# Performance work log

Hardware: AMD Instinct MI355X
Metric: run time of the kernel (lower is better)

## Reference

```python
import jax, jax.numpy as jnp
import numpy as np
from itertools import permutations

BLOCK = 64  # GroupLinear block_size


def _dist_bucket_table():
    # replicates self.distance: log2-style bucketing of token distances [0,1024)
    t = np.zeros(1024, dtype=np.int32)
    for i, th in enumerate([2, 4, 8, 16, 32, 64, 128, 256, 512]):
        t[th:] = i + 1
    return jnp.asarray(t)


def setup_inputs() -> dict:
    key = jax.random.key(0)
    ks = jax.random.split(key, 12)
    B, S, H, NH = 4, 512, 768, 12
    E, TAG, TE, TD, R = 24, 7, 20, 20, 97
    DIN = 2 * H + TE + TD
    hidden_state = jax.random.normal(ks[0], (B, S, H), jnp.float32)
    attention = jax.random.uniform(ks[1], (B, NH, S, S), jnp.float32)
    attention_mask = jnp.ones((B, S), jnp.float32)
    head = jnp.sort(jax.random.randint(ks[2], (B, E), 0, S), axis=-1)
    tail = jnp.sort(jax.random.randint(ks[3], (B, E), 0, S), axis=-1)
    entity_type = jax.random.randint(ks[4], (B, E), 0, TAG)
    type_table = jax.random.normal(ks[5], (TAG, TE), jnp.float32) * 0.02
    dis_table = jax.random.normal(ks[6], (20, TD), jnp.float32) * 0.02
    Wh = jax.random.normal(ks[7], (DIN, H), jnp.float32) * (1.0 / np.sqrt(DIN))
    bh = jnp.zeros((H,), jnp.float32)
    Wt = jax.random.normal(ks[8], (DIN, H), jnp.float32) * (1.0 / np.sqrt(DIN))
    bt = jnp.zeros((H,), jnp.float32)
    # GroupLinear weight reshaped to [n_blocks, BLOCK, BLOCK, R]
    clsW = jax.random.normal(ks[9], (H // BLOCK, BLOCK, BLOCK, R), jnp.float32) * (1.0 / np.sqrt(H * BLOCK))
    clsb = jnp.zeros((R,), jnp.float32)
    return dict(hidden_state=hidden_state, attention=attention,
                attention_mask=attention_mask, head=head, tail=tail,
                entity_type=entity_type, type_table=type_table,
                dis_table=dis_table, Wh=Wh, bh=bh, Wt=Wt, bt=bt,
                clsW=clsW, clsb=clsb)


def reference(hidden_state, attention, attention_mask, head, tail, entity_type,
              type_table, dis_table, Wh, bh, Wt, bt, clsW, clsb):
    E = head.shape[1]
    hts = jnp.asarray(list(permutations(range(E), 2)), dtype=jnp.int32)  # [P,2]
    i0, i1 = hts[:, 0], hts[:, 1]
    dtab = _dist_bucket_table()
    att = attention.sum(axis=1)  # [B,S,S] sum over heads

    def per_sample(h, a, m, hd, tl, et):
        # h:[S,H] a:[S,S] m:[S] hd,tl,et:[E]
        ent_feat = (h[hd] + h[tl]) * 0.5          # [E,H]
        ent_att = (a[hd] + a[tl]) * 0.5           # [E,S]
        ent_tf = type_table[et]                   # [E,TE]
        head_f, tail_f = ent_feat[i0], ent_feat[i1]      # [P,H]
        ht_att = ent_att[i0] * ent_att[i1] * m[None, :]  # [P,S]
        head_ty, tail_ty = ent_tf[i0], ent_tf[i1]        # [P,TE]
        d = dtab[jnp.abs(tl[i0] - hd[i1])]               # [P]
        ht_dist = dis_table[d]                           # [P,TD]
        ht_att = ht_att / (ht_att.sum(-1, keepdims=True) + 1e-20)
        ht_info = ht_att @ h                             # [P,H]
        all_h = jnp.concatenate([head_f, ht_info, head_ty, ht_dist], axis=-1)
        all_t = jnp.concatenate([tail_f, ht_info, tail_ty, ht_dist], axis=-1)
        return all_h, all_t

    all_h, all_t = jax.vmap(per_sample)(hidden_state, att, attention_mask,
                                        head, tail, entity_type)
    all_h = all_h.reshape(-1, all_h.shape[-1])  # [B*P, DIN]
    all_t = all_t.reshape(-1, all_t.shape[-1])
    h1 = jnp.tanh(all_h @ Wh + bh)              # [L,H]
    t1 = jnp.tanh(all_t @ Wt + bt)
    L, H = h1.shape
    nb = H // BLOCK
    x1 = h1.reshape(L, nb, BLOCK)
    x2 = t1.reshape(L, nb, BLOCK)
    # GroupLinear: per-block outer product then linear, fused as einsum
    logits = jnp.einsum('lnb,lnc,nbcr->lr', x1, x2, clsW) + clsb  # [L,R]
    return logits
```

## Files before the change

### kernel.cpp

```cpp
#include <hip/hip_runtime.h>
#include <hip/hip_bf16.h>
#include <math.h>

#define B_ 4
#define S_ 512
#define H_ 768
#define NH_ 12
#define E_ 24
#define TE_ 20
#define TD_ 20
#define R_ 97
#define DIN_ 1576
#define KPAD_ 1600
#define KS_MLP 50
#define MF_MLP 140
#define KS_HTI 16
#define P_ 552
#define L_ 2208
#define NB_ 12
#define NF_ 7

typedef __bf16 bf16x8 __attribute__((ext_vector_type(8)));
typedef float f32x4 __attribute__((ext_vector_type(4)));

__device__ __forceinline__ unsigned short f2bf(float f) {
  union { float f; unsigned u; } c; c.f = f;
  unsigned r = c.u + 0x7FFF + ((c.u >> 16) & 1);
  return (unsigned short)(r >> 16);
}
__device__ __forceinline__ float bf2f(unsigned short b) {
  union { unsigned u; float f; } c; c.u = ((unsigned)b) << 16;
  return c.f;
}
__device__ __forceinline__ unsigned pk2(float a, float b) {
  return (unsigned)f2bf(a) | ((unsigned)f2bf(b) << 16);
}
__device__ __forceinline__ void gload_lds16(const uint4* g, uint4* l) {
  __builtin_amdgcn_global_load_lds(
      (const __attribute__((address_space(1))) unsigned*)(const void*)g,
      (__attribute__((address_space(3))) unsigned*)(void*)l, 16, 0, 0);
}

__global__ void ent_prep(const float* __restrict__ attn, const float* __restrict__ hs,
                         const int* __restrict__ head, const int* __restrict__ tail,
                         float* __restrict__ ent_att, float* __restrict__ ent_feat) {
  int be = blockIdx.x;
  int b = be / E_;
  int hd = head[be], tl = tail[be];
  int tid = threadIdx.x;
  const float* abase = attn + (size_t)b * NH_ * S_ * S_;
  for (int s = tid; s < S_; s += 256) {
    float acc = 0.f;
#pragma unroll
    for (int nh = 0; nh < NH_; ++nh) {
      const float* ap = abase + (size_t)nh * S_ * S_;
      acc += ap[(size_t)hd * S_ + s] + ap[(size_t)tl * S_ + s];
    }
    ent_att[(size_t)be * S_ + s] = 0.5f * acc;
  }
  const float* hb = hs + (size_t)b * S_ * H_;
  for (int k = tid; k < H_; k += 256) {
    ent_feat[(size_t)be * H_ + k] = 0.5f * (hb[(size_t)hd * H_ + k] + hb[(size_t)tl * H_ + k]);
  }
}

__global__ void pair_att(const float* __restrict__ ent_att, const float* __restrict__ mask,
                         const int* __restrict__ head, const int* __restrict__ tail,
                         const int* __restrict__ etype,
                         float* __restrict__ ht_att, int* __restrict__ meta) {
  int l = blockIdx.x;
  int b = l / P_, p = l % P_;
  int i0 = p / (E_ - 1), rem = p % (E_ - 1);
  int i1 = rem + (rem >= i0 ? 1 : 0);
  int tid = threadIdx.x;
  if (tid == 0) {
    meta[0 * L_ + l] = b * E_ + i0;
    meta[1 * L_ + l] = b * E_ + i1;
    meta[2 * L_ + l] = etype[b * E_ + i0];
    meta[3 * L_ + l] = etype[b * E_ + i1];
    int d = abs(tail[b * E_ + i0] - head[b * E_ + i1]);
    int bk = (d >= 2) + (d >= 4) + (d >= 8) + (d >= 16) + (d >= 32) +
             (d >= 64) + (d >= 128) + (d >= 256) + (d >= 512);
    meta[4 * L_ + l] = bk;
  }
  const float* a0 = ent_att + (size_t)(b * E_ + i0) * S_;
  const float* a1 = ent_att + (size_t)(b * E_ + i1) * S_;
  const float* m = mask + (size_t)b * S_;
  float v0 = a0[tid] * a1[tid] * m[tid];
  float v1 = a0[tid + 256] * a1[tid + 256] * m[tid + 256];
  float loc = v0 + v1;
  for (int o = 32; o > 0; o >>= 1) loc += __shfl_down(loc, o, 64);
  __shared__ float red[4];
  if ((tid & 63) == 0) red[tid >> 6] = loc;
  __syncthreads();
  float tot = red[0] + red[1] + red[2] + red[3];
  float inv = 1.f / (tot + 1e-20f);
  ht_att[(size_t)l * S_ + tid] = v0 * inv;
  ht_att[(size_t)l * S_ + tid + 256] = v1 * inv;
}

__global__ void pack_hs(const float* __restrict__ hs, uint4* __restrict__ hsP) {
  int u = blockIdx.x * 256 + threadIdx.x;
  if (u >= B_ * KS_HTI * 48 * 64) return;
  int lane = u & 63;
  int t = u >> 6;
  int nt16 = t % 48;
  int t2 = t / 48;
  int ks = t2 % KS_HTI;
  int b = t2 / KS_HTI;
  int n = nt16 * 16 + (lane & 15);
  int k0 = ks * 32 + ((lane >> 4) << 3);
  const float* src = hs + (size_t)b * S_ * H_;
  unsigned w[4];
#pragma unroll
  for (int q = 0; q < 4; ++q) {
    int k = k0 + 2 * q;
    w[q] = pk2(src[(size_t)k * H_ + n], src[(size_t)(k + 1) * H_ + n]);
  }
  uint4 o; o.x = w[0]; o.y = w[1]; o.z = w[2]; o.w = w[3];
  hsP[u] = o;
}

__global__ void pack_Wmlp(const float* __restrict__ Wh, const float* __restrict__ Wt,
                          uint4* __restrict__ WpH, uint4* __restrict__ WpT) {
  int u = blockIdx.x * 256 + threadIdx.x;
  if (u >= KS_MLP * 48 * 64) return;
  const float* W = blockIdx.y ? Wt : Wh;
  uint4* Wp = blockIdx.y ? WpT : WpH;
  int lane = u & 63;
  int t = u >> 6;
  int nt16 = t % 48;
  int ks = t / 48;
  int n = nt16 * 16 + (lane & 15);
  int k0 = ks * 32 + ((lane >> 4) << 3);
  unsigned w[4];
#pragma unroll
  for (int q = 0; q < 4; ++q) {
    int k = k0 + 2 * q;
    float v0 = (k < DIN_) ? W[(size_t)k * H_ + n] : 0.f;
    float v1 = (k + 1 < DIN_) ? W[(size_t)(k + 1) * H_ + n] : 0.f;
    w[q] = pk2(v0, v1);
  }
  uint4 o; o.x = w[0]; o.y = w[1]; o.z = w[2]; o.w = w[3];
  Wp[u] = o;
}

__global__ void pack_allx(const float* __restrict__ ent_feat, const float* __restrict__ ht_info,
                          const float* __restrict__ ttab, const float* __restrict__ dtab,
                          const int* __restrict__ meta,
                          uint4* __restrict__ axH, uint4* __restrict__ axT) {
  int idx = blockIdx.x * 256 + threadIdx.x;
  int lane = idx & 63;
  int unit = idx >> 6;
  int half = unit / (MF_MLP * KS_MLP);
  int rem = unit % (MF_MLP * KS_MLP);
  int mf = rem / KS_MLP, ks = rem % KS_MLP;
  int row = mf * 16 + (lane & 15);
  int k = ks * 32 + ((lane >> 4) << 3);
  uint4 d; d.x = d.y = d.z = d.w = 0;
  if (row < L_) {
    int frow = meta[half * L_ + row];
    int trow = meta[(2 + half) * L_ + row];
    int db = meta[4 * L_ + row];
    if (k < 768) {
      const float* p = ent_feat + (size_t)frow * H_ + k;
      float4 v0 = *(const float4*)p, v1 = *(const float4*)(p + 4);
      d.x = pk2(v0.x, v0.y); d.y = pk2(v0.z, v0.w);
      d.z = pk2(v1.x, v1.y); d.w = pk2(v1.z, v1.w);
    } else if (k < 1536) {
      const float* p = ht_info + (size_t)row * H_ + (k - 768);
      float4 v0 = *(const float4*)p, v1 = *(const float4*)(p + 4);
      d.x = pk2(v0.x, v0.y); d.y = pk2(v0.z, v0.w);
      d.z = pk2(v1.x, v1.y); d.w = pk2(v1.z, v1.w);
    } else {
      float v[8];
#pragma unroll
      for (int j = 0; j < 8; ++j) {
        int e = k + j;
        v[j] = (e < 1556) ? ttab[trow * TE_ + (e - 1536)]
             : (e < 1576) ? dtab[db * TD_ + (e - 1556)] : 0.f;
      }
      d.x = pk2(v[0], v[1]); d.y = pk2(v[2], v[3]);
      d.z = pk2(v[4], v[5]); d.w = pk2(v[6], v[7]);
    }
  }
  (half ? axT : axH)[(size_t)rem * 64 + lane] = d;
}

__global__ __launch_bounds__(256) void htinfo_mfma(
    const float* __restrict__ htatt, const uint4* __restrict__ hsP,
    float* __restrict__ htinfo) {
  int b = blockIdx.z;
  int m0 = blockIdx.x * 64;
  int nt0 = blockIdx.y * 4;
  int tid = threadIdx.x;
  int wave = tid >> 6, lane = tid & 63;
  int wm = wave & 1, wn = wave >> 1;
  __shared__ __align__(16) uint4 Ash[2][512];
  __shared__ __align__(16) uint4 Bsh[2][512];

  f32x4 acc[2][2];
#pragma unroll
  for (int i = 0; i < 2; ++i)
#pragma unroll
    for (int j = 0; j < 2; ++j) acc[i][j] = (f32x4){0.f, 0.f, 0.f, 0.f};

  auto stageB = [&](int s, int buf) {
#pragma unroll
    for (int i = 0; i < 2; ++i) {
      int c = wave * 2 + i;
      int ntl = c >> 1, kslot = c & 1;
      gload_lds16(hsP + ((size_t)(b * KS_HTI + s * 2 + kslot) * 48 + nt0 + ntl) * 64 + lane,
                  &Bsh[buf][c * 64]);
    }
  };
  auto gatherA = [&](int s, int c, uint4& d) {
    int mfl = c >> 1, kslot = c & 1;
    int row = m0 + mfl * 16 + (lane & 15);
    if (row >= P_) { d.x = d.y = d.z = d.w = 0; return; }
    int k = s * 64 + kslot * 32 + ((lane >> 4) << 3);
    const float* p = htatt + ((size_t)b * P_ + row) * S_ + k;
    float4 v0 = *(const float4*)p, v1 = *(const float4*)(p + 4);
    d.x = pk2(v0.x, v0.y); d.y = pk2(v0.z, v0.w);
    d.z = pk2(v1.x, v1.y); d.w = pk2(v1.z, v1.w);
  };

  {
    uint4 a0_, a1_;
    gatherA(0, wave, a0_); gatherA(0, wave + 4, a1_);
    Ash[0][wave * 64 + lane] = a0_;
    Ash[0][(wave + 4) * 64 + lane] = a1_;
    stageB(0, 0);
  }
  __syncthreads();

  for (int s = 0; s < 8; ++s) {
    int cur = s & 1, nxt = cur ^ 1;
    bool more = (s + 1 < 8);
    uint4 aN0, aN1;
    if (more) {
      stageB(s + 1, nxt);
      gatherA(s + 1, wave, aN0); gatherA(s + 1, wave + 4, aN1);
    }
    bf16x8 af[2][2], bf[2][2];
#pragma unroll
    for (int mf = 0; mf < 2; ++mf)
#pragma unroll
      for (int kc = 0; kc < 2; ++kc)
        af[mf][kc] = *(const bf16x8*)&Ash[cur][((wm * 2 + mf) * 2 + kc) * 64 + lane];
#pragma unroll
    for (int nf = 0; nf < 2; ++nf)
#pragma unroll
      for (int kc = 0; kc < 2; ++kc)
        bf[nf][kc] = *(const bf16x8*)&Bsh[cur][((wn * 2 + nf) * 2 + kc) * 64 + lane];
#pragma unroll
    for (int kc = 0; kc < 2; ++kc)
#pragma unroll
      for (int nf = 0; nf < 2; ++nf)
#pragma unroll
        for (int mf = 0; mf < 2; ++mf)
          acc[mf][nf] = __builtin_amdgcn_mfma_f32_16x16x32_bf16(af[mf][kc], bf[nf][kc], acc[mf][nf], 0, 0, 0);
    if (more) {
      Ash[nxt][wave * 64 + lane] = aN0;
      Ash[nxt][(wave + 4) * 64 + lane] = aN1;
    }
    __syncthreads();
  }

#pragma unroll
  for (int mf = 0; mf < 2; ++mf)
#pragma unroll
    for (int nf = 0; nf < 2; ++nf) {
      int n = nt0 * 16 + (wn * 2 + nf) * 16 + (lane & 15);
#pragma unroll
      for (int reg = 0; reg < 4; ++reg) {
        int l = m0 + (wm * 2 + mf) * 16 + ((lane >> 4) << 2) + reg;
        if (l < P_)
          htinfo[((size_t)b * P_ + l) * H_ + n] = acc[mf][nf][reg];
      }
    }
}

__global__ __launch_bounds__(256) void mlp_mfma(
    const uint4* __restrict__ Apk_h, const uint4* __restrict__ Apk_t,
    const uint4* __restrict__ Wp_h, const uint4* __restrict__ Wp_t,
    const float* __restrict__ bh, const float* __restrict__ bt,
    float* __restrict__ h1, float* __restrict__ t1) {
  int half = blockIdx.z;
  const uint4* Apk = half ? Apk_t : Apk_h;
  const uint4* Wp = half ? Wp_t : Wp_h;
  const float* bias = half ? bt : bh;
  float* out = half ? t1 : h1;
  int mf0 = blockIdx.x * 4;
  int nt0 = blockIdx.y * 4;
  int tid = threadIdx.x;
  int wave = tid >> 6, lane = tid & 63;
  int wm = wave & 1, wn = wave >> 1;
  __shared__ __align__(16) uint4 Ash[2][512];
  __shared__ __align__(16) uint4 Bsh[2][512];

  f32x4 acc[2][2];
#pragma unroll
  for (int i = 0; i < 2; ++i)
#pragma unroll
    for (int j = 0; j < 2; ++j) acc[i][j] = (f32x4){0.f, 0.f, 0.f, 0.f};

  auto stage = [&](int s, int buf) {
#pragma unroll
    for (int i = 0; i < 2; ++i) {
      int c = wave * 2 + i;
      int cl = c >> 1, kslot = c & 1;
      gload_lds16(Apk + ((size_t)(mf0 + cl) * KS_MLP + s * 2 + kslot) * 64 + lane,
                  &Ash[buf][c * 64]);
      gload_lds16(Wp + ((size_t)(s * 2 + kslot) * 48 + nt0 + cl) * 64 + lane,
                  &Bsh[buf][c * 64]);
    }
  };

  stage(0, 0);
  __syncthreads();

  for (int s = 0; s < 25; ++s) {
    int cur = s & 1, nxt = cur ^ 1;
    if (s + 1 < 25) stage(s + 1, nxt);
    bf16x8 af[2][2], bf[2][2];
#pragma unroll
    for (int mf = 0; mf < 2; ++mf)
#pragma unroll
      for (int kc = 0; kc < 2; ++kc)
        af[mf][kc] = *(const bf16x8*)&Ash[cur][((wm * 2 + mf) * 2 + kc) * 64 + lane];
#pragma unroll
    for (int nf = 0; nf < 2; ++nf)
#pragma unroll
      for (int kc = 0; kc < 2; ++kc)
        bf[nf][kc] = *(const bf16x8*)&Bsh[cur][((wn * 2 + nf) * 2 + kc) * 64 + lane];
#pragma unroll
    for (int kc = 0; kc < 2; ++kc)
#pragma unroll
      for (int nf = 0; nf < 2; ++nf)
#pragma unroll
        for (int mf = 0; mf < 2; ++mf)
          acc[mf][nf] = __builtin_amdgcn_mfma_f32_16x16x32_bf16(af[mf][kc], bf[nf][kc], acc[mf][nf], 0, 0, 0);
    __syncthreads();
  }

#pragma unroll
  for (int mf = 0; mf < 2; ++mf)
#pragma unroll
    for (int nf = 0; nf < 2; ++nf) {
      int n = nt0 * 16 + (wn * 2 + nf) * 16 + (lane & 15);
      float bv = bias[n];
#pragma unroll
      for (int reg = 0; reg < 4; ++reg) {
        int l = (mf0 + wm * 2 + mf) * 16 + ((lane >> 4) << 2) + reg;
        if (l < L_)
          out[(size_t)l * H_ + n] = tanhf(acc[mf][nf][reg] + bv);
      }
    }
}

__global__ void pack_w(const float* __restrict__ clsW, uint4* __restrict__ Wfrag) {
  int nb = blockIdx.x;
  __shared__ float Wls[64][98];
  int tid = threadIdx.x;
  const float* src = clsW + (size_t)nb * 64 * R_;
  for (int idx = tid; idx < 64 * R_; idx += 256) {
    Wls[idx / R_][idx % R_] = src[idx];
  }
  __syncthreads();
  for (int u = tid; u < 896; u += 256) {
    int nf = u >> 7;
    int kc = (u >> 6) & 1;
    int lane = u & 63;
    int r = (lane & 15) + 16 * nf;
    unsigned w[4];
#pragma unroll
    for (int q = 0; q < 4; ++q) {
      int c0 = ((lane >> 4) << 3) + 2 * q + 32 * kc;
      float v0 = (r < R_) ? Wls[c0][r] : 0.f;
      float v1 = (r < R_) ? Wls[c0 + 1][r] : 0.f;
      w[q] = (unsigned)f2bf(v0) | ((unsigned)f2bf(v1) << 16);
    }
    uint4 o; o.x = w[0]; o.y = w[1]; o.z = w[2]; o.w = w[3];
    Wfrag[(size_t)nb * 896 + u] = o;
  }
}

__global__ __launch_bounds__(256) void bilinear_mfma(
    const float* __restrict__ h1, const float* __restrict__ t1,
    const uint4* __restrict__ Wfrag, float* __restrict__ part,
    float* __restrict__ part2) {
  int n = blockIdx.y;
  int z = blockIdx.z;
  int l0 = blockIdx.x * 64;
  int tid = threadIdx.x;
  int wave = tid >> 6, lane = tid & 63;
  int wm = wave & 1, kh = wave >> 1;
  __shared__ __align__(16) uint4 Wl[2][2][896];
  __shared__ unsigned short x1s[64][64];

  for (int i = tid; i < 1024; i += 256) {
    int l = i >> 4, bq = (i & 15) * 4;
    float4 v = make_float4(0, 0, 0, 0);
    if (l0 + l < L_) v = *(const float4*)(h1 + (size_t)(l0 + l) * H_ + n * 64 + bq);
    x1s[bq + 0][l] = f2bf(v.x);
    x1s[bq + 1][l] = f2bf(v.y);
    x1s[bq + 2][l] = f2bf(v.z);
    x1s[bq + 3][l] = f2bf(v.w);
  }

  float x2f[2][2][8];
#pragma unroll
  for (int mf = 0; mf < 2; ++mf) {
    int row = l0 + wm * 32 + mf * 16 + (lane & 15);
#pragma unroll
    for (int kc = 0; kc < 2; ++kc) {
      float4 v0 = make_float4(0, 0, 0, 0), v1 = v0;
      if (row < L_) {
        const float* p = t1 + (size_t)row * H_ + n * 64 + kc * 32 + ((lane >> 4) << 3);
        v0 = *(const float4*)p;
        v1 = *(const float4*)(p + 4);
      }
      x2f[mf][kc][0] = v0.x; x2f[mf][kc][1] = v0.y;
      x2f[mf][kc][2] = v0.z; x2f[mf][kc][3] = v0.w;
      x2f[mf][kc][4] = v1.x; x2f[mf][kc][5] = v1.y;
      x2f[mf][kc][6] = v1.z; x2f[mf][kc][7] = v1.w;
    }
  }

  f32x4 acc[2][NF_];
#pragma unroll
  for (int mf = 0; mf < 2; ++mf)
#pragma unroll
    for (int nf = 0; nf < NF_; ++nf)
      acc[mf][nf] = (f32x4){0.f, 0.f, 0.f, 0.f};

  const uint4* gbase = Wfrag + (size_t)n * 64 * 896;
  auto stage = [&](int b, int buf) {
    const uint4* gs = gbase + (size_t)b * 896 + (wm * 7) * 64 + lane;
#pragma unroll
    for (int r = 0; r < 7; ++r)
      gload_lds16(gs + r * 64, &Wl[kh][buf][(wm * 7 + r) * 64]);
  };

  int bstart = z * 32 + kh * 16;
  stage(bstart, 0);
  __syncthreads();

  for (int s = 0; s < 16; ++s) {
    int b = bstart + s;
    int cur = s & 1, nxt = cur ^ 1;
    if (s + 1 < 16) stage(b + 1, nxt);
    bf16x8 afr[2][2];
#pragma unroll
    for (int mf = 0; mf < 2; ++mf) {
      float x1v = bf2f(x1s[b][wm * 32 + mf * 16 + (lane & 15)]);
#pragma unroll
      for (int kc = 0; kc < 2; ++kc)
#pragma unroll
        for (int j = 0; j < 8; ++j)
          afr[mf][kc][j] = (__bf16)(x1v * x2f[mf][kc][j]);
    }
#pragma unroll
    for (int nf = 0; nf < NF_; ++nf) {
#pragma unroll
      for (int kc = 0; kc < 2; ++kc) {
        bf16x8 bfr = *(const bf16x8*)&Wl[kh][cur][(nf * 2 + kc) * 64 + lane];
#pragma unroll
        for (int mf = 0; mf < 2; ++mf)
          acc[mf][nf] = __builtin_amdgcn_mfma_f32_16x16x32_bf16(
              afr[mf][kc], bfr, acc[mf][nf], 0, 0, 0);
      }
    }
    __syncthreads();
  }

  float* red = (float*)&Wl[0][0][0];
  int rbase = (wm * 64 + lane) * 68;
  if (kh == 1) {
#pragma unroll
    for (int mf = 0; mf < 2; ++mf)
#pragma unroll
      for (int nf = 0; nf < NF_; ++nf)
        *(f32x4*)&red[rbase + (mf * NF_ + nf) * 4] = acc[mf][nf];
  }
  __syncthreads();
  if (kh == 0) {
    float* dst = (z == 0) ? part : part2;
#pragma unroll
    for (int mf = 0; mf < 2; ++mf)
#pragma unroll
      for (int nf = 0; nf < NF_; ++nf)
        acc[mf][nf] += *(const f32x4*)&red[rbase + (mf * NF_ + nf) * 4];
#pragma unroll
    for (int mf = 0; mf < 2; ++mf) {
#pragma unroll
      for (int nf = 0; nf < NF_; ++nf) {
        int r = nf * 16 + (lane & 15);
        if (r < R_) {
#pragma unroll
          for (int reg = 0; reg < 4; ++reg) {
            int l = l0 + wm * 32 + mf * 16 + ((lane >> 4) << 2) + reg;
            if (l < L_)
              dst[((size_t)n * L_ + l) * R_ + r] = acc[mf][nf][reg];
          }
        }
      }
    }
  }
}

__global__ void reduce_logits(const float* __restrict__ part, const float* __restrict__ part2,
                              const float* __restrict__ clsb, float* __restrict__ out) {
  int idx = blockIdx.x * 256 + threadIdx.x;
  if (idx < L_ * R_) {
    int r = idx % R_;
    float s = clsb[r];
#pragma unroll
    for (int nn = 0; nn < NB_; ++nn)
      s += part[(size_t)nn * L_ * R_ + idx] + part2[(size_t)nn * L_ * R_ + idx];
    out[idx] = s;
  }
}

extern "C" void kernel_launch(void* const* d_in, const int* in_sizes, int n_in,
                              void* d_out, int out_size, void* d_ws, size_t ws_size,
                              hipStream_t stream) {
  const float* hs   = (const float*)d_in[0];
  const float* attn = (const float*)d_in[1];
  const float* mask = (const float*)d_in[2];
  const int*   head = (const int*)d_in[3];
  const int*   tail = (const int*)d_in[4];
  const int*   etyp = (const int*)d_in[5];
  const float* ttab = (const float*)d_in[6];
  const float* dtab = (const float*)d_in[7];
  const float* Wh   = (const float*)d_in[8];
  const float* bh   = (const float*)d_in[9];
  const float* Wt   = (const float*)d_in[10];
  const float* bt   = (const float*)d_in[11];
  const float* clsW = (const float*)d_in[12];
  const float* clsb = (const float*)d_in[13];
  float* out = (float*)d_out;

  float* ws = (float*)d_ws;
  float* ent_att  = ws; ws += (size_t)B_ * E_ * S_;
  float* ent_feat = ws; ws += (size_t)B_ * E_ * H_;
  float* ht_att   = ws; ws += (size_t)L_ * S_;
  float* ht_info  = ws; ws += (size_t)L_ * H_;
  float* h1       = ws; ws += (size_t)L_ * H_;
  float* t1       = ws; ws += (size_t)L_ * H_;
  float* part     = ws; ws += (size_t)NB_ * L_ * R_;
  uint4* Wpack_h  = (uint4*)ws; ws += (size_t)KS_MLP * 48 * 64 * 4;
  uint4* Wpack_t  = (uint4*)ws; ws += (size_t)KS_MLP * 48 * 64 * 4;
  uint4* hsPack   = (uint4*)ws; ws += (size_t)B_ * KS_HTI * 48 * 64 * 4;
  uint4* Wfrag    = (uint4*)ws; ws += (size_t)NB_ * 64 * 896 * 4;
  uint4* allx_h   = (uint4*)ws; ws += (size_t)MF_MLP * KS_MLP * 64 * 4;
  uint4* allx_t   = (uint4*)ws; ws += (size_t)MF_MLP * KS_MLP * 64 * 4;
  int* meta = (int*)ws;
  float* part2 = (float*)allx_h;

  ent_prep<<<B_ * E_, 256, 0, stream>>>(attn, hs, head, tail, ent_att, ent_feat);
  pair_att<<<L_, 256, 0, stream>>>(ent_att, mask, head, tail, etyp, ht_att, meta);
  pack_hs<<<(B_ * KS_HTI * 48 * 64) / 256, 256, 0, stream>>>(hs, hsPack);
  htinfo_mfma<<<dim3(9, 12, B_), 256, 0, stream>>>(ht_att, hsPack, ht_info);
  pack_Wmlp<<<dim3((KS_MLP * 48 * 64) / 256, 2), 256, 0, stream>>>(Wh, Wt, Wpack_h, Wpack_t);
  pack_allx<<<(2 * MF_MLP * KS_MLP * 64) / 256, 256, 0, stream>>>(
      ent_feat, ht_info, ttab, dtab, meta, allx_h, allx_t);
  mlp_mfma<<<dim3(35, 12, 2), 256, 0, stream>>>(allx_h, allx_t,
      Wpack_h, Wpack_t, bh, bt, h1, t1);
  pack_w<<<NB_ * 64, 256, 0, stream>>>(clsW, Wfrag);
  bilinear_mfma<<<dim3(35, NB_, 2), 256, 0, stream>>>(h1, t1, Wfrag, part, part2);
  reduce_logits<<<(L_ * R_ + 255) / 256, 256, 0, stream>>>(part, part2, clsb, out);
}
```

Measured before the change: 133.4 us.

## Enlarge bilinear row tile to 256 and drop intra-block K split

The bilinear MFMA kernel now assigns 256 rows per block (64 per wave, four M fragments each) instead of 64. Each wave walks all 32 K-steps itself, which removes the two-way K split and its LDS reduction. Each staged weight fragment is now reused across four times as many rows, cutting weight traffic and the number of blocks. The grid shrinks from 840 to 216 blocks, and each wave holds more accumulator registers and runs a longer serial loop, so latency hiding and CU occupancy may drop.

```diff
diff --git a/kernel.cpp b/kernel.cpp
--- a/kernel.cpp
+++ b/kernel.cpp
@@ -386,20 +386,19 @@
   }
 }
 
-__global__ __launch_bounds__(256) void bilinear_mfma(
+__global__ __launch_bounds__(256, 2) void bilinear_mfma(
     const float* __restrict__ h1, const float* __restrict__ t1,
     const uint4* __restrict__ Wfrag, float* __restrict__ part,
     float* __restrict__ part2) {
   int n = blockIdx.y;
   int z = blockIdx.z;
-  int l0 = blockIdx.x * 64;
+  int l0 = blockIdx.x * 256;
   int tid = threadIdx.x;
   int wave = tid >> 6, lane = tid & 63;
-  int wm = wave & 1, kh = wave >> 1;
-  __shared__ __align__(16) uint4 Wl[2][2][896];
-  __shared__ unsigned short x1s[64][64];
-
-  for (int i = tid; i < 1024; i += 256) {
+  __shared__ __align__(16) uint4 Wl[2][896];
+  __shared__ unsigned short x1s[64][256];
+
+  for (int i = tid; i < 4096; i += 256) {
     int l = i >> 4, bq = (i & 15) * 4;
     float4 v = make_float4(0, 0, 0, 0);
     if (l0 + l < L_) v = *(const float4*)(h1 + (size_t)(l0 + l) * H_ + n * 64 + bq);
@@ -409,10 +408,10 @@
     x1s[bq + 3][l] = f2bf(v.w);
   }
 
-  float x2f[2][2][8];
-#pragma unroll
-  for (int mf = 0; mf < 2; ++mf) {
-    int row = l0 + wm * 32 + mf * 16 + (lane & 15);
+  float x2f[4][2][8];
+#pragma unroll
+  for (int mf = 0; mf < 4; ++mf) {
+    int row = l0 + wave * 64 + mf * 16 + (lane & 15);
 #pragma unroll
     for (int kc = 0; kc < 2; ++kc) {
       float4 v0 = make_float4(0, 0, 0, 0), v1 = v0;
@@ -428,33 +427,35 @@
     }
   }
 
-  f32x4 acc[2][NF_];
-#pragma unroll
-  for (int mf = 0; mf < 2; ++mf)
+  f32x4 acc[4][NF_];
+#pragma unroll
+  for (int mf = 0; mf < 4; ++mf)
 #pragma unroll
     for (int nf = 0; nf < NF_; ++nf)
       acc[mf][nf] = (f32x4){0.f, 0.f, 0.f, 0.f};
 
   const uint4* gbase = Wfrag + (size_t)n * 64 * 896;
   auto stage = [&](int b, int buf) {
-    const uint4* gs = gbase + (size_t)b * 896 + (wm * 7) * 64 + lane;
-#pragma unroll
-    for (int r = 0; r < 7; ++r)
-      gload_lds16(gs + r * 64, &Wl[kh][buf][(wm * 7 + r) * 64]);
+    const uint4* gs = gbase + (size_t)b * 896;
+#pragma unroll
+    for (int r = 0; r < 3; ++r)
+      gload_lds16(gs + (wave * 3 + r) * 64 + lane, &Wl[buf][(wave * 3 + r) * 64]);
+    if (wave < 2)
+      gload_lds16(gs + 768 + wave * 64 + lane, &Wl[buf][768 + wave * 64]);
   };
 
-  int bstart = z * 32 + kh * 16;
+  int bstart = z * 32;
   stage(bstart, 0);
   __syncthreads();
 
-  for (int s = 0; s < 16; ++s) {
+  for (int s = 0; s < 32; ++s) {
     int b = bstart + s;
     int cur = s & 1, nxt = cur ^ 1;
-    if (s + 1 < 16) stage(b + 1, nxt);
-    bf16x8 afr[2][2];
-#pragma unroll
-    for (int mf = 0; mf < 2; ++mf) {
-      float x1v = bf2f(x1s[b][wm * 32 + mf * 16 + (lane & 15)]);
+    if (s + 1 < 32) stage(b + 1, nxt);
+    bf16x8 afr[4][2];
+#pragma unroll
+    for (int mf = 0; mf < 4; ++mf) {
+      float x1v = bf2f(x1s[b][wave * 64 + mf * 16 + (lane & 15)]);
 #pragma unroll
       for (int kc = 0; kc < 2; ++kc)
 #pragma unroll
@@ -465,9 +466,9 @@
     for (int nf = 0; nf < NF_; ++nf) {
 #pragma unroll
       for (int kc = 0; kc < 2; ++kc) {
-        bf16x8 bfr = *(const bf16x8*)&Wl[kh][cur][(nf * 2 + kc) * 64 + lane];
-#pragma unroll
-        for (int mf = 0; mf < 2; ++mf)
+        bf16x8 bfr = *(const bf16x8*)&Wl[cur][(nf * 2 + kc) * 64 + lane];
+#pragma unroll
+        for (int mf = 0; mf < 4; ++mf)
           acc[mf][nf] = __builtin_amdgcn_mfma_f32_16x16x32_bf16(
               afr[mf][kc], bfr, acc[mf][nf], 0, 0, 0);
       }
@@ -475,35 +476,18 @@
     __syncthreads();
   }
 
-  float* red = (float*)&Wl[0][0][0];
-  int rbase = (wm * 64 + lane) * 68;
-  if (kh == 1) {
-#pragma unroll
-    for (int mf = 0; mf < 2; ++mf)
-#pragma unroll
-      for (int nf = 0; nf < NF_; ++nf)
-        *(f32x4*)&red[rbase + (mf * NF_ + nf) * 4] = acc[mf][nf];
-  }
-  __syncthreads();
-  if (kh == 0) {
-    float* dst = (z == 0) ? part : part2;
-#pragma unroll
-    for (int mf = 0; mf < 2; ++mf)
-#pragma unroll
-      for (int nf = 0; nf < NF_; ++nf)
-        acc[mf][nf] += *(const f32x4*)&red[rbase + (mf * NF_ + nf) * 4];
-#pragma unroll
-    for (int mf = 0; mf < 2; ++mf) {
-#pragma unroll
-      for (int nf = 0; nf < NF_; ++nf) {
-        int r = nf * 16 + (lane & 15);
-        if (r < R_) {
-#pragma unroll
-          for (int reg = 0; reg < 4; ++reg) {
-            int l = l0 + wm * 32 + mf * 16 + ((lane >> 4) << 2) + reg;
-            if (l < L_)
-              dst[((size_t)n * L_ + l) * R_ + r] = acc[mf][nf][reg];
-          }
+  float* dst = (z == 0) ? part : part2;
+#pragma unroll
+  for (int mf = 0; mf < 4; ++mf) {
+#pragma unroll
+    for (int nf = 0; nf < NF_; ++nf) {
+      int r = nf * 16 + (lane & 15);
+      if (r < R_) {
+#pragma unroll
+        for (int reg = 0; reg < 4; ++reg) {
+          int l = l0 + wave * 64 + mf * 16 + ((lane >> 4) << 2) + reg;
+          if (l < L_)
+            dst[((size_t)n * L_ + l) * R_ + r] = acc[mf][nf][reg];
         }
       }
     }
@@ -569,6 +553,6 @@
   mlp_mfma<<<dim3(35, 12, 2), 256, 0, stream>>>(allx_h, allx_t,
       Wpack_h, Wpack_t, bh, bt, h1, t1);
   pack_w<<<NB_ * 64, 256, 0, stream>>>(clsW, Wfrag);
-  bilinear_mfma<<<dim3(35, NB_, 2), 256, 0, stream>>>(h1, t1, Wfrag, part, part2);
+  bilinear_mfma<<<dim3(9, NB_, 2), 256, 0, stream>>>(h1, t1, Wfrag, part, part2);
   reduce_logits<<<(L_ * R_ + 255) / 256, 256, 0, stream>>>(part, part2, clsb, out);
 }
```

After: 136.9 us. 2.7% more time.

## Remap bilinear blocks per XCD and halve the per-stage LDS footprint

Applied to the files above, without the earlier changes.

The 3D grid of the bilinear kernel becomes a flat 864-block grid. Each XCD (blk&7) is assigned fixed (n, z) weight slices so that blocks sharing the same Wfrag slice land on the same L2. The LDS pipeline now stages one k-chunk per step (7 fragments instead of 14) over 32 steps. Only the 32 x1 columns this z-half needs are loaded, which shrinks LDS use and may allow more resident blocks. The trade-off is twice as many barriers, plus one extra bounds-checked row tile per (n, z) pair, since 36 tiles cover 35 needed.

```diff
diff --git a/kernel.cpp b/kernel.cpp
--- a/kernel.cpp
+++ b/kernel.cpp
@@ -390,23 +390,29 @@
     const float* __restrict__ h1, const float* __restrict__ t1,
     const uint4* __restrict__ Wfrag, float* __restrict__ part,
     float* __restrict__ part2) {
-  int n = blockIdx.y;
-  int z = blockIdx.z;
-  int l0 = blockIdx.x * 64;
+  int blk = blockIdx.x;
+  int xcd = blk & 7;
+  int slot = blk >> 3;
+  int pg = slot / 36;
+  int j = slot % 36;
+  int p = pg * 8 + xcd;
+  int n = p >> 1, z = p & 1;
+  int l0 = j * 64;
   int tid = threadIdx.x;
   int wave = tid >> 6, lane = tid & 63;
   int wm = wave & 1, kh = wave >> 1;
-  __shared__ __align__(16) uint4 Wl[2][2][896];
-  __shared__ unsigned short x1s[64][64];
-
-  for (int i = tid; i < 1024; i += 256) {
-    int l = i >> 4, bq = (i & 15) * 4;
+  __shared__ __align__(16) uint4 Wl[2][2][7][64];
+  __shared__ unsigned short x1s[32][66];
+
+  for (int i = tid; i < 512; i += 256) {
+    int row = i >> 3, cq = (i & 7) * 4;
     float4 v = make_float4(0, 0, 0, 0);
-    if (l0 + l < L_) v = *(const float4*)(h1 + (size_t)(l0 + l) * H_ + n * 64 + bq);
-    x1s[bq + 0][l] = f2bf(v.x);
-    x1s[bq + 1][l] = f2bf(v.y);
-    x1s[bq + 2][l] = f2bf(v.z);
-    x1s[bq + 3][l] = f2bf(v.w);
+    if (l0 + row < L_)
+      v = *(const float4*)(h1 + (size_t)(l0 + row) * H_ + n * 64 + z * 32 + cq);
+    x1s[cq + 0][row] = f2bf(v.x);
+    x1s[cq + 1][row] = f2bf(v.y);
+    x1s[cq + 2][row] = f2bf(v.z);
+    x1s[cq + 3][row] = f2bf(v.w);
   }
 
   float x2f[2][2][8];
@@ -417,9 +423,9 @@
     for (int kc = 0; kc < 2; ++kc) {
       float4 v0 = make_float4(0, 0, 0, 0), v1 = v0;
       if (row < L_) {
-        const float* p = t1 + (size_t)row * H_ + n * 64 + kc * 32 + ((lane >> 4) << 3);
-        v0 = *(const float4*)p;
-        v1 = *(const float4*)(p + 4);
+        const float* ptr = t1 + (size_t)row * H_ + n * 64 + kc * 32 + ((lane >> 4) << 3);
+        v0 = *(const float4*)ptr;
+        v1 = *(const float4*)(ptr + 4);
       }
       x2f[mf][kc][0] = v0.x; x2f[mf][kc][1] = v0.y;
       x2f[mf][kc][2] = v0.z; x2f[mf][kc][3] = v0.w;
@@ -436,47 +442,50 @@
       acc[mf][nf] = (f32x4){0.f, 0.f, 0.f, 0.f};
 
   const uint4* gbase = Wfrag + (size_t)n * 64 * 896;
-  auto stage = [&](int b, int buf) {
-    const uint4* gs = gbase + (size_t)b * 896 + (wm * 7) * 64 + lane;
-#pragma unroll
-    for (int r = 0; r < 7; ++r)
-      gload_lds16(gs + r * 64, &Wl[kh][buf][(wm * 7 + r) * 64]);
+  auto stage = [&](int s, int buf) {
+    int b = z * 32 + kh * 16 + (s >> 1);
+    int kc = s & 1;
+    const uint4* gs = gbase + (size_t)b * 896 + kc * 64 + lane;
+    if (wm == 0) {
+#pragma unroll
+      for (int nf = 0; nf < 4; ++nf)
+        gload_lds16(gs + nf * 128, &Wl[kh][buf][nf][0]);
+    } else {
+#pragma unroll
+      for (int nf = 4; nf < 7; ++nf)
+        gload_lds16(gs + nf * 128, &Wl[kh][buf][nf][0]);
+    }
   };
 
-  int bstart = z * 32 + kh * 16;
-  stage(bstart, 0);
+  stage(0, 0);
   __syncthreads();
 
-  for (int s = 0; s < 16; ++s) {
-    int b = bstart + s;
+  for (int s = 0; s < 32; ++s) {
     int cur = s & 1, nxt = cur ^ 1;
-    if (s + 1 < 16) stage(b + 1, nxt);
-    bf16x8 afr[2][2];
+    if (s + 1 < 32) stage(s + 1, nxt);
+    int bl = kh * 16 + (s >> 1);
+    int kc = s & 1;
+    bf16x8 afr[2];
 #pragma unroll
     for (int mf = 0; mf < 2; ++mf) {
-      float x1v = bf2f(x1s[b][wm * 32 + mf * 16 + (lane & 15)]);
-#pragma unroll
-      for (int kc = 0; kc < 2; ++kc)
-#pragma unroll
-        for (int j = 0; j < 8; ++j)
-          afr[mf][kc][j] = (__bf16)(x1v * x2f[mf][kc][j]);
+      float x1v = bf2f(x1s[bl][wm * 32 + mf * 16 + (lane & 15)]);
+#pragma unroll
+      for (int jj = 0; jj < 8; ++jj)
+        afr[mf][jj] = (__bf16)(x1v * x2f[mf][kc][jj]);
     }
 #pragma unroll
     for (int nf = 0; nf < NF_; ++nf) {
-#pragma unroll
-      for (int kc = 0; kc < 2; ++kc) {
-        bf16x8 bfr = *(const bf16x8*)&Wl[kh][cur][(nf * 2 + kc) * 64 + lane];
-#pragma unroll
-        for (int mf = 0; mf < 2; ++mf)
-          acc[mf][nf] = __builtin_amdgcn_mfma_f32_16x16x32_bf16(
-              afr[mf][kc], bfr, acc[mf][nf], 0, 0, 0);
-      }
+      bf16x8 bfr = *(const bf16x8*)&Wl[kh][cur][nf][lane];
+#pragma unroll
+      for (int mf = 0; mf < 2; ++mf)
+        acc[mf][nf] = __builtin_amdgcn_mfma_f32_16x16x32_bf16(
+            afr[mf], bfr, acc[mf][nf], 0, 0, 0);
     }
     __syncthreads();
   }
 
-  float* red = (float*)&Wl[0][0][0];
-  int rbase = (wm * 64 + lane) * 68;
+  float* red = (float*)&Wl[0][0][0][0];
+  int rbase = (wm * 64 + lane) * 56;
   if (kh == 1) {
 #pragma unroll
     for (int mf = 0; mf < 2; ++mf)
@@ -488,14 +497,10 @@
   if (kh == 0) {
     float* dst = (z == 0) ? part : part2;
 #pragma unroll
-    for (int mf = 0; mf < 2; ++mf)
-#pragma unroll
-      for (int nf = 0; nf < NF_; ++nf)
+    for (int mf = 0; mf < 2; ++mf) {
+#pragma unroll
+      for (int nf = 0; nf < NF_; ++nf) {
         acc[mf][nf] += *(const f32x4*)&red[rbase + (mf * NF_ + nf) * 4];
-#pragma unroll
-    for (int mf = 0; mf < 2; ++mf) {
-#pragma unroll
-      for (int nf = 0; nf < NF_; ++nf) {
         int r = nf * 16 + (lane & 15);
         if (r < R_) {
 #pragma unroll
@@ -569,6 +574,6 @@
   mlp_mfma<<<dim3(35, 12, 2), 256, 0, stream>>>(allx_h, allx_t,
       Wpack_h, Wpack_t, bh, bt, h1, t1);
   pack_w<<<NB_ * 64, 256, 0, stream>>>(clsW, Wfrag);
-  bilinear_mfma<<<dim3(35, NB_, 2), 256, 0, stream>>>(h1, t1, Wfrag, part, part2);
+  bilinear_mfma<<<864, 256, 0, stream>>>(h1, t1, Wfrag, part, part2);
   reduce_logits<<<(L_ * R_ + 255) / 256, 256, 0, stream>>>(part, part2, clsb, out);
 }
```

Result: faster. 127.5 us (-4.4%).
